# Kernel tuning notes

Hardware: AMD Instinct MI355X
Metric: run time of the kernel (lower is better)

Reference implementation:

```python
import jax, jax.numpy as jnp
import numpy as np

B, SY, SX, CIN = 16, 180, 360, 16
WIDTH, MODES = 32, 32


def _vandermonde(pos, modes):
    # Nonuniform DFT matrix V[k, n] = exp(-2*pi*i * k * p_n) / sqrt(L),
    # positions normalized to [0, 1). Inverse uses conj(V) (near-unitary).
    p = (pos - pos.min()) / (pos.max() - pos.min())
    k = jnp.arange(modes, dtype=jnp.float32)
    V = jnp.exp(-2j * jnp.pi * k[:, None] * p[None, :]) / jnp.sqrt(jnp.float32(pos.shape[0]))
    return V.astype(jnp.complex64)


def _spectral(h, fw1, fw2, Vy, Vx):
    # h: [B, C, M, N]; Vy: [modes, M]; Vx: [modes, N]
    hc = h.astype(jnp.complex64)
    w1 = fw1[..., 0] + 1j * fw1[..., 1]  # [I, O, modes] complex
    w2 = fw2[..., 0] + 1j * fw2[..., 1]
    # y-direction: forward transform over M, mix channels per mode, inverse
    fty = jnp.einsum('bimn,km->bink', hc, Vy)          # [B, I, N, modes]
    oy = jnp.einsum('bink,iok->bonk', fty, w1)          # [B, O, N, modes]
    xy = jnp.einsum('bonk,km->bomn', oy, jnp.conj(Vy)).real
    # x-direction: forward transform over N
    ftx = jnp.einsum('bimn,kn->bimk', hc, Vx)           # [B, I, M, modes]
    ox = jnp.einsum('bimk,iok->bomk', ftx, w2)          # [B, O, M, modes]
    xx = jnp.einsum('bomk,kn->bomn', ox, jnp.conj(Vx)).real
    return xx + xy


def gelu(v):
    return jax.nn.gelu(v, approximate=False)  # torch F.gelu default (erf)


def setup_inputs() -> dict:
    key = jax.random.key(0)
    ks = jax.random.split(key, 16)
    s = 1.0 / (WIDTH * WIDTH)
    return {
        'x': jax.random.normal(ks[0], (B, SY, SX, CIN), jnp.float32),
        'sparse_x': jnp.sort(jax.random.uniform(ks[1], (SX,), jnp.float32)),
        'sparse_y': jnp.sort(jax.random.uniform(ks[2], (SY,), jnp.float32)),
        'fc0_w': jax.random.normal(ks[3], (CIN + 2, WIDTH), jnp.float32) * 0.1,
        'fc0_b': jnp.zeros((WIDTH,), jnp.float32),
        'fw1': jax.random.uniform(ks[4], (4, WIDTH, WIDTH, MODES, 2), jnp.float32) * s,
        'fw2': jax.random.uniform(ks[5], (4, WIDTH, WIDTH, MODES, 2), jnp.float32) * s,
        'w1': jax.random.normal(ks[6], (4, WIDTH, WIDTH), jnp.float32) * 0.1,
        'b1': jnp.zeros((4, WIDTH), jnp.float32),
        'w2': jax.random.normal(ks[7], (4, WIDTH, WIDTH), jnp.float32) * 0.1,
        'b2': jnp.zeros((4, WIDTH), jnp.float32),
        'fc1_w': jax.random.normal(ks[8], (WIDTH, 128), jnp.float32) * 0.1,
        'fc1_b': jnp.zeros((128,), jnp.float32),
        'fc2_w': jax.random.normal(ks[9], (128, 1), jnp.float32) * 0.1,
        'fc2_b': jnp.zeros((1,), jnp.float32),
    }


def reference(x, sparse_x, sparse_y, fc0_w, fc0_b, fw1, fw2, w1, b1, w2, b2,
              fc1_w, fc1_b, fc2_w, fc2_b):
    b, sy, sx, _ = x.shape
    # get_grid (faithful to source: (p - min)/max)
    gx = (sparse_x - sparse_x.min()) / sparse_x.max()          # [SX]
    gy = (sparse_y - sparse_y.min()) / sparse_y.max()          # [SY]
    grid = jnp.stack([jnp.broadcast_to(gx[None, :], (sy, sx)),
                      jnp.broadcast_to(gy[:, None], (sy, sx))], axis=-1)
    grid = jnp.broadcast_to(grid[None], (b, sy, sx, 2))
    h = jnp.concatenate([x, grid], axis=-1) @ fc0_w + fc0_b    # [B, SY, SX, W]
    h = jnp.transpose(h, (0, 3, 1, 2))                         # [B, W, SY, SX]

    Vy = _vandermonde(sparse_y, MODES)
    Vx = _vandermonde(sparse_x, MODES)

    for i in range(4):
        x1 = _spectral(h, fw1[i], fw2[i], Vy, Vx)
        x2 = jnp.einsum('bcmn,oc->bomn', x1, w1[i]) + b1[i][None, :, None, None]
        x4 = jnp.einsum('bcmn,oc->bomn', gelu(x2), w2[i]) + b2[i][None, :, None, None]
        h = (gelu(x4) if i < 3 else x4) + h  # last block: no gelu on x4 (per source)

    h = jnp.transpose(h, (0, 2, 3, 1))                         # [B, SY, SX, W]
    h = gelu(h @ fc1_w + fc1_b)
    return h @ fc2_w + fc2_b                                   # [B, SY, SX, 1]
```

## Files before the change

### kernel.cpp

```cpp
#include <hip/hip_runtime.h>
#include <math.h>

#define NB 16
#define NSY 180
#define NSX 360
#define NCIN 16
#define NW 32
#define NMODES 32
#define NPIX (NSY*NSX)
#define NPTS (NB*NPIX)

typedef unsigned int uint;
typedef unsigned short ushort;
typedef __attribute__((ext_vector_type(8))) short bf16x8;
typedef __attribute__((ext_vector_type(4))) float f32x4;

union U4 { uint u[4]; bf16x8 v; };

__device__ __forceinline__ float gelu_f(float v){
  float u = v*(-2.3021681f - 0.10295335f*v*v);
  return v * __builtin_amdgcn_rcpf(1.f + exp2f(u));
}
__device__ __forceinline__ ushort f2bf(float x){
  uint u = __float_as_uint(x);
  return (ushort)((u + 0x7FFFu + ((u>>16)&1u)) >> 16);
}
__device__ __forceinline__ uint packbf2(float a, float b){
  return (uint)f2bf(a) | ((uint)f2bf(b) << 16);
}
__device__ __forceinline__ float bf2f(ushort u){
  return __uint_as_float(((uint)u) << 16);
}
__device__ __forceinline__ uint addbf2(uint h, uint a){
  return packbf2(bf2f((ushort)(h & 0xffffu)) + bf2f((ushort)(a & 0xffffu)),
                 bf2f((ushort)(h >> 16))     + bf2f((ushort)(a >> 16)));
}

__global__ __launch_bounds__(256) void k_prep(const float* __restrict__ sx,
    const float* __restrict__ sy, const float* __restrict__ fc1_w,
    const float* __restrict__ w2m,
    ushort* __restrict__ Abfy, ushort* __restrict__ Abfx,
    ushort* __restrict__ VyCT, ushort* __restrict__ VxCT,
    ushort* __restrict__ f1Tbf, ushort* __restrict__ w2bf,
    float* __restrict__ gx, float* __restrict__ gy){
  int idx = blockIdx.x*256 + threadIdx.x;
  float sx0 = sx[0], sxL = sx[NSX-1];
  float sy0 = sy[0], syL = sy[NSY-1];
  const float scy = 0.07453559924999298980f;
  const float scx = 0.05270462766947298886f;
  if (idx < NSX) gx[idx] = (sx[idx]-sx0)/sxL;
  if (idx < NSY) gy[idx] = (sy[idx]-sy0)/syL;
  if (idx < 64*192){
    int kri = idx/192, m = idx%192;
    float val = 0.f;
    if (m < NSY){
      int k = kri>>1;
      float p = (sy[m]-sy0)/(syL-sy0);
      float ang = -6.2831853071795864769f*(float)k*p;
      val = ((kri&1)? sinf(ang) : cosf(ang))*scy;
    }
    Abfy[idx] = f2bf(val);
  }
  if (idx < 192*64){
    int m = idx/64, kri = idx%64;
    float val = 0.f;
    if (m < NSY){
      int k = kri>>1;
      float p = (sy[m]-sy0)/(syL-sy0);
      float ang = -6.2831853071795864769f*(float)k*p;
      val = ((kri&1)? sinf(ang) : cosf(ang))*scy;
    }
    VyCT[idx] = f2bf(val);
  }
  if (idx < 64*384){
    int kri = idx/384, n = idx%384;
    float val = 0.f;
    if (n < NSX){
      int k = kri>>1;
      float p = (sx[n]-sx0)/(sxL-sx0);
      float ang = -6.2831853071795864769f*(float)k*p;
      val = ((kri&1)? sinf(ang) : cosf(ang))*scx;
    }
    Abfx[idx] = f2bf(val);
  }
  if (idx < 384*64){
    int n = idx/64, kri = idx%64;
    float val = 0.f;
    if (n < NSX){
      int k = kri>>1;
      float p = (sx[n]-sx0)/(sxL-sx0);
      float ang = -6.2831853071795864769f*(float)k*p;
      val = ((kri&1)? sinf(ang) : cosf(ang))*scx;
    }
    VxCT[idx] = f2bf(val);
  }
  if (idx < 128*32){
    int j = idx >> 5, c = idx & 31;
    f1Tbf[idx] = f2bf(fc1_w[c*128 + j]);
  }
  if (idx < 4096){
    w2bf[idx] = f2bf(w2m[idx]);
  }
}

__global__ __launch_bounds__(256) void k_fold(const float* __restrict__ fw1,
    const float* __restrict__ fw2, const float* __restrict__ w1m,
    float* __restrict__ w1f, float* __restrict__ w2f){
  int id = blockIdx.x*256 + threadIdx.x;
  int half = id >> 17;
  int r = id & 131071;
  int i  = r >> 15;
  int in = (r >> 10) & 31;
  int k  = (r >> 5) & 31;
  int o  = r & 31;
  const float* src = half ? fw2 : fw1;
  const float* wm  = w1m + i*1024 + o*32;
  const float* sp  = src + ((size_t)((i*32+in)*1024 + k))*2;
  float sR = 0.f, sI = 0.f;
  #pragma unroll
  for (int c=0;c<32;c++){
    float w = wm[c];
    sR += w * sp[c*64];
    sI += w * sp[c*64+1];
  }
  float* dst = half ? w2f : w1f;
  size_t oi = ((size_t)((i*32+in)*32 + k)*32 + o)*2;
  dst[oi] = sR; dst[oi+1] = sI;
}

__global__ __launch_bounds__(256) void k_fc0(const float* __restrict__ x,
    const float* __restrict__ gx, const float* __restrict__ gy,
    const float* __restrict__ fw, const float* __restrict__ fb,
    ushort* __restrict__ hbf){
  int p = blockIdx.x*256 + threadIdx.x;
  if (p >= NPTS) return;
  int b = p/NPIX, r = p%NPIX, m = r/NSX, n = r%NSX;
  const float* xp = x + (size_t)p*NCIN;
  float xv[NCIN+2];
  #pragma unroll
  for (int j=0;j<NCIN;j++) xv[j] = xp[j];
  xv[16] = gx[n]; xv[17] = gy[m];
  float acc[NW];
  #pragma unroll
  for (int o=0;o<NW;o++) acc[o] = fb[o];
  #pragma unroll
  for (int j=0;j<NCIN+2;j++){
    float v = xv[j];
    #pragma unroll
    for (int o=0;o<NW;o++) acc[o] += v*fw[j*32+o];
  }
  ushort* hq = hbf + (size_t)b*NW*NPIX + r;
  #pragma unroll
  for (int o=0;o<NW;o++) hq[(size_t)o*NPIX] = f2bf(acc[o]);
}

__global__ __launch_bounds__(256) void k_fwd(const ushort* __restrict__ hbf,
    const ushort* __restrict__ Abfy, const ushort* __restrict__ Abfx,
    uint* __restrict__ fty, uint* __restrict__ ftx, int b0, int ylim){
  __shared__ ushort rawS[2][32*64];
  __shared__ uint   BtS[2][64*18];
  int bx = blockIdx.x;
  int tid = threadIdx.x;
  int l = tid & 63, g = tid >> 6;
  int c15 = l & 15, q = l >> 4;
  if (bx < ylim){
    int nt6 = bx % 6; int c = (bx/6) & 31; int bb = bx/192;
    int n0 = nt6*64;
    const ushort* hb = hbf + (size_t)((b0+bb)*NW + c)*NPIX;
    int yr = tid >> 3, yc = (tid & 7) << 3;
    auto ldY = [&](int ks)->uint4{
      int m = ks*32 + yr;
      int gc = n0 + yc;
      uint4 p = {0u,0u,0u,0u};
      if (m < NSY && gc < NSX) p = *(const uint4*)(hb + (size_t)m*NSX + gc);
      return p;
    };
    bf16x8 afr[6];
    #pragma unroll
    for (int ks=0; ks<6; ks++)
      afr[ks] = *(const bf16x8*)(Abfy + (size_t)(16*g + c15)*192 + ks*32 + q*8);
    f32x4 acc[4];
    #pragma unroll
    for (int t=0;t<4;t++) acc[t] = (f32x4){0.f,0.f,0.f,0.f};
    uint4 pre0 = ldY(0);
    uint4 pre1 = ldY(1);
    #pragma unroll
    for (int ks=0; ks<6; ks++){
      uint4 cur = (ks&1) ? pre1 : pre0;
      *(uint4*)(&rawS[ks&1][(size_t)tid*8]) = cur;
      __syncthreads();
      if (ks < 4){
        if (ks&1) pre1 = ldY(ks+2); else pre0 = ldY(ks+2);
      }
      const ushort* rp = rawS[ks&1];
      ushort v[8];
      #pragma unroll
      for (int j=0;j<8;j++) v[j] = rp[(8*g + j)*64 + l];
      #pragma unroll
      for (int i=0;i<4;i++)
        BtS[ks&1][l*18 + 4*g + i] = (uint)v[2*i] | ((uint)v[2*i+1] << 16);
      __syncthreads();
      #pragma unroll
      for (int nt=0; nt<4; nt++){
        const uint* bp = &BtS[ks&1][(nt*16 + c15)*18 + q*4];
        U4 bu;
        uint2 lo = *(const uint2*)(bp);
        uint2 hi = *(const uint2*)(bp+2);
        bu.u[0]=lo.x; bu.u[1]=lo.y; bu.u[2]=hi.x; bu.u[3]=hi.y;
        acc[nt] = __builtin_amdgcn_mfma_f32_16x16x32_bf16(afr[ks], bu.v, acc[nt], 0,0,0);
      }
    }
    uint* fb = fty + (size_t)(bb*NW + c)*32*NSX;
    int k0 = 8*g + 2*q;
    #pragma unroll
    for (int nt=0; nt<4; nt++){
      int nn = n0 + nt*16 + c15;
      if (nn < NSX){
        fb[(size_t)k0*NSX + nn]     = packbf2(acc[nt][0], acc[nt][1]);
        fb[(size_t)(k0+1)*NSX + nn] = packbf2(acc[nt][2], acc[nt][3]);
      }
    }
  } else {
    int t = bx - ylim;
    int mt = t % 3; int c = (t/3) & 31; int bb = t/96;
    int m0 = mt*64;
    const ushort* hb = hbf + (size_t)((b0+bb)*NW + c)*NPIX;
    int xr = tid >> 2, xc = (tid & 3) << 3;
    auto ldX = [&](int ks)->uint4{
      int m = m0 + xr;
      int n = ks*32 + xc;
      uint4 p = {0u,0u,0u,0u};
      if (m < NSY && n < NSX) p = *(const uint4*)(hb + (size_t)m*NSX + n);
      return p;
    };
    auto ldA = [&](int ks)->bf16x8{
      return *(const bf16x8*)(Abfx + (size_t)(16*g + c15)*384 + ks*32 + q*8);
    };
    f32x4 acc[4];
    #pragma unroll
    for (int tt=0;tt<4;tt++) acc[tt] = (f32x4){0.f,0.f,0.f,0.f};
    uint4 pre0 = ldX(0), pre1 = ldX(1);
    bf16x8 a0 = ldA(0), a1 = ldA(1);
    int s4 = (tid & 3) * 4;
    #pragma unroll
    for (int ks=0; ks<12; ks++){
      uint4 cur = (ks&1) ? pre1 : pre0;
      bf16x8 af = (ks&1) ? a1 : a0;
      uint* btp = &BtS[ks&1][xr*18 + s4];
      btp[0] = cur.x; btp[1] = cur.y; btp[2] = cur.z; btp[3] = cur.w;
      if (ks < 10){
        if (ks&1){ pre1 = ldX(ks+2); a1 = ldA(ks+2); }
        else     { pre0 = ldX(ks+2); a0 = ldA(ks+2); }
      }
      __syncthreads();
      #pragma unroll
      for (int nt=0; nt<4; nt++){
        const uint* bp = &BtS[ks&1][(nt*16 + c15)*18 + q*4];
        U4 bu;
        uint2 lo = *(const uint2*)(bp);
        uint2 hi = *(const uint2*)(bp+2);
        bu.u[0]=lo.x; bu.u[1]=lo.y; bu.u[2]=hi.x; bu.u[3]=hi.y;
        acc[nt] = __builtin_amdgcn_mfma_f32_16x16x32_bf16(af, bu.v, acc[nt], 0,0,0);
      }
    }
    uint* fb = ftx + (size_t)(bb*NW + c)*32*NSY;
    int k0 = 8*g + 2*q;
    #pragma unroll
    for (int nt=0; nt<4; nt++){
      int mm = m0 + nt*16 + c15;
      if (mm < NSY){
        fb[(size_t)k0*NSY + mm]     = packbf2(acc[nt][0], acc[nt][1]);
        fb[(size_t)(k0+1)*NSY + mm] = packbf2(acc[nt][2], acc[nt][3]);
      }
    }
  }
}

__global__ __launch_bounds__(192) void k_mix(const uint* __restrict__ fty,
    const uint* __restrict__ ftx, const float* __restrict__ w1f,
    const float* __restrict__ w2f, uint* __restrict__ oy, uint* __restrict__ ox,
    int ylim){
  int bx = blockIdx.x;
  const uint* ft; const float* wf; uint* oo; int Nlen, k, bb, n;
  if (bx < ylim){
    int t = bx; int nt = t & 1; k = (t>>1) & 31; bb = t >> 6;
    n = nt*192 + threadIdx.x; ft = fty; wf = w1f; oo = oy; Nlen = NSX;
  } else {
    int t = bx - ylim; k = t & 31; bb = t >> 5;
    n = threadIdx.x; ft = ftx; wf = w2f; oo = ox; Nlen = NSY;
  }
  bool valid = n < Nlen;
  int nn = valid ? n : (Nlen-1);
  const uint* fb = ft + ((size_t)(bb*NW)*32 + k)*Nlen + nn;
  const float* wb = wf + (size_t)k*64;
  float aR[32], aI[32];
  #pragma unroll
  for (int o=0;o<32;o++){ aR[o]=0.f; aI[o]=0.f; }
  for (int in=0; in<32; in++){
    uint f = fb[(size_t)in*32*Nlen];
    float fR = bf2f((ushort)(f & 0xffffu));
    float fI = bf2f((ushort)(f >> 16));
    const float* wrow = wb + in*2048;
    #pragma unroll
    for (int o=0;o<32;o++){
      float wR = wrow[o*2], wI = wrow[o*2+1];
      aR[o] += fR*wR - fI*wI;
      aI[o] += fR*wI + fI*wR;
    }
  }
  if (valid){
    uint* ob = oo + ((size_t)(bb*NW)*32 + k)*Nlen + n;
    #pragma unroll
    for (int o=0;o<32;o++){
      ob[(size_t)o*32*Nlen] = packbf2(aR[o], aI[o]);
    }
  }
}

__global__ __launch_bounds__(256) void k_inv(const uint* __restrict__ oyb,
    const uint* __restrict__ oxb, const ushort* __restrict__ VyCT,
    const ushort* __restrict__ VxCT, const float* __restrict__ b1,
    ushort* __restrict__ x2bf){
  __shared__ uint Bt[64*34];
  int bx = blockIdx.x;
  int c8 = bx & 7; int rr = bx >> 3; int slot = rr/6; int nt6 = rr - slot*6;
  int gid = slot*8 + c8;
  int bb = gid >> 5; int o = gid & 31;
  int n0 = nt6*64;
  int tid = threadIdx.x;
  int l = tid & 63, g = tid >> 6;
  int c15 = l & 15, q = l >> 4;
  const uint* oxp = oxb + (size_t)(bb*NW + o)*32*NSY;
  const uint* oyp = oyb + (size_t)(bb*NW + o)*32*NSX;
  #pragma unroll
  for (int i=0;i<8;i++){
    int idx = tid + i*256;
    int k = idx >> 6, n = idx & 63;
    int ng = n0 + n;
    Bt[n*34 + k] = (ng < NSX) ? oyp[(size_t)k*NSX + ng] : 0u;
  }
  __syncthreads();
  f32x4 acc[3][4];
  #pragma unroll
  for (int mt=0;mt<3;mt++)
    #pragma unroll
    for (int nt=0;nt<4;nt++) acc[mt][nt] = (f32x4){0.f,0.f,0.f,0.f};
  #pragma unroll
  for (int s=0;s<4;s++){
    bf16x8 bfr[4];
    #pragma unroll
    for (int nt=0;nt<4;nt++){
      if (s < 2){
        const uint* bp = &Bt[(nt*16 + c15)*34 + s*16 + q*4];
        U4 bu; uint2 lo = *(const uint2*)bp; uint2 hi = *(const uint2*)(bp+2);
        bu.u[0]=lo.x; bu.u[1]=lo.y; bu.u[2]=hi.x; bu.u[3]=hi.y;
        bfr[nt] = bu.v;
      } else {
        bfr[nt] = *(const bf16x8*)(VxCT + (size_t)(n0 + nt*16 + c15)*64 + (s-2)*32 + q*8);
      }
    }
    #pragma unroll
    for (int mt=0;mt<3;mt++){
      int mrow = g*48 + mt*16 + c15;
      bf16x8 afr;
      if (s < 2){
        afr = *(const bf16x8*)(VyCT + (size_t)mrow*64 + s*32 + q*8);
      } else {
        int mc = mrow < NSY ? mrow : (NSY-1);
        int k0 = (s-2)*16 + q*4;
        U4 au;
        #pragma unroll
        for (int j=0;j<4;j++)
          au.u[j] = oxp[(size_t)(k0+j)*NSY + mc];
        afr = au.v;
      }
      #pragma unroll
      for (int nt=0;nt<4;nt++)
        acc[mt][nt] = __builtin_amdgcn_mfma_f32_16x16x32_bf16(afr, bfr[nt], acc[mt][nt], 0,0,0);
    }
  }
  float bias = b1[o];
  ushort* xp = x2bf + (size_t)(bb*NW + o)*NPIX;
  #pragma unroll
  for (int mt=0;mt<3;mt++){
    #pragma unroll
    for (int nt=0;nt<4;nt++){
      int n = n0 + nt*16 + c15;
      if (n < NSX){
        #pragma unroll
        for (int r2=0;r2<4;r2++){
          int m = g*48 + mt*16 + q*4 + r2;
          if (m < NSY) xp[(size_t)m*NSX + n] = f2bf(gelu_f(acc[mt][nt][r2] + bias));
        }
      }
    }
  }
}

__global__ __launch_bounds__(256) void k_pw2(const ushort* __restrict__ x2bf,
    const ushort* __restrict__ w2b, const float* __restrict__ b2,
    uint* __restrict__ hbfu, int b0, int nloc){
  const int HP = NPIX/2;
  __shared__ uint Ot[32*132];
  int blk = blockIdx.x;
  int bb = blk/254, bt = blk - bb*254;
  int pxb = bt*256;
  int tid = threadIdx.x;
  int g = tid >> 6, l = tid & 63;
  int c15 = l & 15, q = l >> 4;
  bf16x8 bfr[2];
  #pragma unroll
  for (int nt=0; nt<2; nt++)
    bfr[nt] = *(const bf16x8*)(w2b + (size_t)(nt*16 + c15)*32 + q*8);
  const ushort* xb = x2bf + ((size_t)bb*NW + q*8)*NPIX;
  f32x4 acc[4][2];
  #pragma unroll
  for (int mt=0;mt<4;mt++){
    U4 au; au.u[0]=0u; au.u[1]=0u; au.u[2]=0u; au.u[3]=0u;
    int pr = pxb + g*64 + mt*16 + c15;
    if (pr < NPIX){
      ushort v[8];
      #pragma unroll
      for (int j=0;j<8;j++) v[j] = xb[(size_t)j*NPIX + pr];
      #pragma unroll
      for (int i2=0;i2<4;i2++) au.u[i2] = (uint)v[2*i2] | ((uint)v[2*i2+1] << 16);
    }
    #pragma unroll
    for (int nt=0;nt<2;nt++){
      acc[mt][nt] = (f32x4){0.f,0.f,0.f,0.f};
      acc[mt][nt] = __builtin_amdgcn_mfma_f32_16x16x32_bf16(au.v, bfr[nt], acc[mt][nt], 0,0,0);
    }
  }
  #pragma unroll
  for (int nt=0;nt<2;nt++){
    int o = nt*16 + c15;
    float bias = b2[o];
    #pragma unroll
    for (int mt=0;mt<4;mt++){
      float v0 = gelu_f(acc[mt][nt][0] + bias);
      float v1 = gelu_f(acc[mt][nt][1] + bias);
      float v2 = gelu_f(acc[mt][nt][2] + bias);
      float v3 = gelu_f(acc[mt][nt][3] + bias);
      int px2 = g*32 + mt*8 + q*2;
      uint2 w2v; w2v.x = packbf2(v0,v1); w2v.y = packbf2(v2,v3);
      *(uint2*)(&Ot[o*132 + px2]) = w2v;
    }
  }
  __syncthreads();
  int o = tid >> 3, t8 = tid & 7;
  uint* hb = hbfu + ((size_t)((b0+bb)*NW + o))*HP + (pxb>>1) + t8*16;
  const uint* lrow = &Ot[o*132 + t8*16];
  int p2g0 = (pxb>>1) + t8*16;
  #pragma unroll
  for (int jj=0; jj<16; jj+=4){
    if (p2g0 + jj + 4 <= HP){
      uint4 hv = *(const uint4*)(hb + jj);
      uint4 av = *(const uint4*)(lrow + jj);
      uint4 r;
      r.x = addbf2(hv.x, av.x); r.y = addbf2(hv.y, av.y);
      r.z = addbf2(hv.z, av.z); r.w = addbf2(hv.w, av.w);
      *(uint4*)(hb + jj) = r;
    } else {
      #pragma unroll
      for (int t=0;t<4;t++){
        if (p2g0 + jj + t < HP){
          uint hv = hb[jj+t];
          hb[jj+t] = addbf2(hv, lrow[jj+t]);
        }
      }
    }
  }
}

__global__ __launch_bounds__(256) void k_pw2f(const ushort* __restrict__ x2bf,
    const ushort* __restrict__ w2b, const float* __restrict__ b2,
    const uint* __restrict__ hbfu,
    const ushort* __restrict__ f1Tbf, const float* __restrict__ f1b,
    const float* __restrict__ f2w, const float* __restrict__ f2b,
    float* __restrict__ out, int b0){
  const int HP = NPIX/2;
  __shared__ uint Ot[32*132];
  int blk = blockIdx.x;
  int bb = blk/254, bt = blk - bb*254;
  int pxb = bt*256;
  int tid = threadIdx.x;
  int g = tid >> 6, l = tid & 63;
  int c15 = l & 15, q = l >> 4;
  bf16x8 bfr[2];
  #pragma unroll
  for (int nt=0; nt<2; nt++)
    bfr[nt] = *(const bf16x8*)(w2b + (size_t)(nt*16 + c15)*32 + q*8);
  const ushort* xb = x2bf + ((size_t)bb*NW + q*8)*NPIX;
  f32x4 acc[4][2];
  #pragma unroll
  for (int mt=0;mt<4;mt++){
    U4 au; au.u[0]=0u; au.u[1]=0u; au.u[2]=0u; au.u[3]=0u;
    int pr = pxb + g*64 + mt*16 + c15;
    if (pr < NPIX){
      ushort v[8];
      #pragma unroll
      for (int j=0;j<8;j++) v[j] = xb[(size_t)j*NPIX + pr];
      #pragma unroll
      for (int i2=0;i2<4;i2++) au.u[i2] = (uint)v[2*i2] | ((uint)v[2*i2+1] << 16);
    }
    #pragma unroll
    for (int nt=0;nt<2;nt++){
      acc[mt][nt] = (f32x4){0.f,0.f,0.f,0.f};
      acc[mt][nt] = __builtin_amdgcn_mfma_f32_16x16x32_bf16(au.v, bfr[nt], acc[mt][nt], 0,0,0);
    }
  }
  #pragma unroll
  for (int nt=0;nt<2;nt++){
    int o = nt*16 + c15;
    float bias = b2[o];
    #pragma unroll
    for (int mt=0;mt<4;mt++){
      float v0 = acc[mt][nt][0] + bias;
      float v1 = acc[mt][nt][1] + bias;
      float v2 = acc[mt][nt][2] + bias;
      float v3 = acc[mt][nt][3] + bias;
      int px2 = g*32 + mt*8 + q*2;
      uint2 w2v; w2v.x = packbf2(v0,v1); w2v.y = packbf2(v2,v3);
      *(uint2*)(&Ot[o*132 + px2]) = w2v;
    }
  }
  __syncthreads();
  {
    int o = tid >> 3, t8 = tid & 7;
    const uint* hb = hbfu + ((size_t)((b0+bb)*NW + o))*HP + (pxb>>1) + t8*16;
    uint* lrow = &Ot[o*132 + t8*16];
    int p2g0 = (pxb>>1) + t8*16;
    #pragma unroll
    for (int jj=0; jj<16; jj+=4){
      if (p2g0 + jj + 4 <= HP){
        uint4 hv = *(const uint4*)(hb + jj);
        lrow[jj+0] = addbf2(hv.x, lrow[jj+0]);
        lrow[jj+1] = addbf2(hv.y, lrow[jj+1]);
        lrow[jj+2] = addbf2(hv.z, lrow[jj+2]);
        lrow[jj+3] = addbf2(hv.w, lrow[jj+3]);
      } else {
        #pragma unroll
        for (int t=0;t<4;t++){
          if (p2g0 + jj + t < HP)
            lrow[jj+t] = addbf2(hb[jj+t], lrow[jj+t]);
        }
      }
    }
  }
  bf16x8 b1fr[8];
  #pragma unroll
  for (int nt=0; nt<8; nt++)
    b1fr[nt] = *(const bf16x8*)(f1Tbf + (size_t)(nt*16 + c15)*32 + q*8);
  __syncthreads();
  const ushort* Ts = (const ushort*)Ot;
  float fb2 = f2b[0];
  float* ob = out + (size_t)(b0+bb)*NPIX + pxb;
  #pragma unroll
  for (int mt=0;mt<4;mt++){
    int px_in = g*64 + mt*16 + c15;
    const ushort* tp = Ts + (size_t)(q*8)*264 + px_in;
    ushort v[8];
    #pragma unroll
    for (int j2=0;j2<8;j2++) v[j2] = tp[j2*264];
    U4 au;
    #pragma unroll
    for (int i2=0;i2<4;i2++) au.u[i2] = (uint)v[2*i2] | ((uint)v[2*i2+1] << 16);
    f32x4 a8[8];
    #pragma unroll
    for (int nt=0; nt<8; nt++){
      a8[nt] = (f32x4){0.f,0.f,0.f,0.f};
      a8[nt] = __builtin_amdgcn_mfma_f32_16x16x32_bf16(au.v, b1fr[nt], a8[nt], 0,0,0);
    }
    float s[4] = {0.f,0.f,0.f,0.f};
    #pragma unroll
    for (int nt=0; nt<8; nt++){
      int jj = nt*16 + c15;
      float bj = f1b[jj], wj = f2w[jj];
      #pragma unroll
      for (int r2=0;r2<4;r2++) s[r2] += gelu_f(a8[nt][r2] + bj) * wj;
    }
    #pragma unroll
    for (int msk=1; msk<16; msk<<=1){
      #pragma unroll
      for (int r2=0;r2<4;r2++) s[r2] += __shfl_xor(s[r2], msk, 64);
    }
    if (c15 == 0){
      int pl = g*64 + mt*16 + q*4;
      if (pxb + pl + 4 <= NPIX){
        float4 o4 = {s[0]+fb2, s[1]+fb2, s[2]+fb2, s[3]+fb2};
        *(float4*)(ob + pl) = o4;
      }
    }
  }
}

extern "C" void kernel_launch(void* const* d_in, const int* in_sizes, int n_in,
                              void* d_out, int out_size, void* d_ws, size_t ws_size,
                              hipStream_t stream) {
  const float* x     = (const float*)d_in[0];
  const float* sx    = (const float*)d_in[1];
  const float* sy    = (const float*)d_in[2];
  const float* fc0_w = (const float*)d_in[3];
  const float* fc0_b = (const float*)d_in[4];
  const float* fw1   = (const float*)d_in[5];
  const float* fw2   = (const float*)d_in[6];
  const float* w1m   = (const float*)d_in[7];
  const float* b1    = (const float*)d_in[8];
  const float* w2m   = (const float*)d_in[9];
  const float* b2    = (const float*)d_in[10];
  const float* fc1_w = (const float*)d_in[11];
  const float* fc1_b = (const float*)d_in[12];
  const float* fc2_w = (const float*)d_in[13];
  const float* fc2_b = (const float*)d_in[14];
  float* out = (float*)d_out;

  char* wsb = (char*)d_ws;
  size_t off = 0;
  auto alloc = [&](size_t bytes)->char*{
    char* p = wsb + off;
    off = (off + bytes + 255) & ~(size_t)255;
    return p;
  };
  ushort* hbf   = (ushort*)alloc((size_t)NB*NW*NPIX*2);
  ushort* Abfy  = (ushort*)alloc(64*192*2);
  ushort* Abfx  = (ushort*)alloc(64*384*2);
  ushort* VyCT  = (ushort*)alloc(192*64*2);
  ushort* VxCT  = (ushort*)alloc(384*64*2);
  ushort* f1Tbf = (ushort*)alloc(128*32*2);
  ushort* w2bf  = (ushort*)alloc(4096*2);
  float*  gx    = (float*)alloc(NSX*4);
  float*  gy    = (float*)alloc(NSY*4);
  float*  w1f   = (float*)alloc(262144*4);
  float*  w2f   = (float*)alloc(262144*4);
  const size_t fixedB = off;

  const size_t szX2  = (size_t)NW*NPIX*2;
  const size_t szFty = (size_t)NW*32*NSX*4;
  const size_t szFtx = (size_t)NW*32*NSY*4;
  const size_t szOy  = szFty, szOx = szFtx;
  const size_t perB  = szX2 + szOy + szOx;

  int NC = 16;
  while (NC > 1 && fixedB + (size_t)NC*perB + 4096 > ws_size) NC >>= 1;
  char* pb = wsb + fixedB;
  ushort* x2bf = (ushort*)pb;
  uint*   fty  = (uint*)pb;
  uint*   ftx  = (uint*)(pb + (size_t)NC*szFty);
  uint*   oy   = (uint*)(pb + (size_t)NC*szX2);
  uint*   ox   = (uint*)((char*)oy + (size_t)NC*szOy);

  k_prep<<<96, 256, 0, stream>>>(sx, sy, fc1_w, w2m, Abfy, Abfx, VyCT, VxCT,
                                 f1Tbf, w2bf, gx, gy);
  k_fold<<<1024, 256, 0, stream>>>(fw1, fw2, w1m, w1f, w2f);
  k_fc0<<<4050, 256, 0, stream>>>(x, gx, gy, fc0_w, fc0_b, hbf);

  for (int i=0;i<4;i++){
    for (int b0=0; b0<NB; b0+=NC){
      k_fwd<<<NC*288, 256, 0, stream>>>(hbf, Abfy, Abfx, fty, ftx, b0, NC*192);
      k_mix<<<NC*96, 192, 0, stream>>>(fty, ftx, w1f + (size_t)i*65536,
                                       w2f + (size_t)i*65536, oy, ox, NC*64);
      k_inv<<<NC*192, 256, 0, stream>>>(oy, ox, VyCT, VxCT, b1 + i*32, x2bf);
      if (i < 3){
        k_pw2<<<NC*254, 256, 0, stream>>>((const ushort*)x2bf,
                                          w2bf + (size_t)i*1024,
                                          b2 + i*32, (uint*)hbf, b0, NC);
      } else {
        k_pw2f<<<NC*254, 256, 0, stream>>>((const ushort*)x2bf,
                                           w2bf + (size_t)i*1024,
                                           b2 + i*32, (const uint*)hbf,
                                           f1Tbf, fc1_b, fc2_w, fc2_b,
                                           out, b0);
      }
    }
  }
}
```

Before: 921.3 us.

## Run spectral channel mixing on bf16 MFMA with split hi/lo weights

Replaces the scalar FP32 complex channel-mix kernel with an MFMA version. The folded weights are pre-packed into bf16 hi/lo pairs arranged as real-valued 2x2 complex blocks, so the mix becomes bf16 matrix multiplies with error-compensated weights. Each block handles all N positions for one (batch, mode) and prefetches the next tile. This is meant to remove the heavy FP32 FMA cost of the per-pixel loops. In exchange it doubles the MFMA count to recover weight precision and changes the weight layout and the launch geometry.

```diff
diff --git a/kernel.cpp b/kernel.cpp
--- a/kernel.cpp
+++ b/kernel.cpp
@@ -105,7 +105,7 @@
 
 __global__ __launch_bounds__(256) void k_fold(const float* __restrict__ fw1,
     const float* __restrict__ fw2, const float* __restrict__ w1m,
-    float* __restrict__ w1f, float* __restrict__ w2f){
+    ushort* __restrict__ wAbf){
   int id = blockIdx.x*256 + threadIdx.x;
   int half = id >> 17;
   int r = id & 131071;
@@ -123,9 +123,15 @@
     sR += w * sp[c*64];
     sI += w * sp[c*64+1];
   }
-  float* dst = half ? w2f : w1f;
-  size_t oi = ((size_t)((i*32+in)*32 + k)*32 + o)*2;
-  dst[oi] = sR; dst[oi+1] = sI;
+  ushort rH = f2bf(sR);  ushort rL = f2bf(sR - bf2f(rH));
+  ushort iH = f2bf(sI);  ushort iL = f2bf(sI - bf2f(iH));
+  ushort nH = f2bf(-sI); ushort nL = f2bf(-sI - bf2f(nH));
+  ushort* base = wAbf + (((size_t)((i*2 + half)*32 + k)) << 13);
+  int oi = o*64 + 2*in;
+  base[oi]          = rH;  base[oi+1]        = nH;
+  base[2048 + oi]   = rL;  base[2048 + oi+1] = nL;
+  base[4096 + oi]   = iH;  base[4096 + oi+1] = rH;
+  base[6144 + oi]   = iL;  base[6144 + oi+1] = rL;
 }
 
 __global__ __launch_bounds__(256) void k_fc0(const float* __restrict__ x,
@@ -276,43 +282,73 @@
   }
 }
 
-__global__ __launch_bounds__(192) void k_mix(const uint* __restrict__ fty,
-    const uint* __restrict__ ftx, const float* __restrict__ w1f,
-    const float* __restrict__ w2f, uint* __restrict__ oy, uint* __restrict__ ox,
-    int ylim){
+__global__ __launch_bounds__(256) void k_mix2(const uint* __restrict__ fty,
+    const uint* __restrict__ ftx, const ushort* __restrict__ wA,
+    uint* __restrict__ oy, uint* __restrict__ ox, int ylim){
   int bx = blockIdx.x;
-  const uint* ft; const float* wf; uint* oo; int Nlen, k, bb, n;
+  const uint* ft; uint* oo; int Nlen, NT, k, bb, halfoff;
   if (bx < ylim){
-    int t = bx; int nt = t & 1; k = (t>>1) & 31; bb = t >> 6;
-    n = nt*192 + threadIdx.x; ft = fty; wf = w1f; oo = oy; Nlen = NSX;
+    bb = bx >> 5; k = bx & 31; ft = fty; oo = oy; Nlen = NSX; NT = 23; halfoff = 0;
   } else {
-    int t = bx - ylim; k = t & 31; bb = t >> 5;
-    n = threadIdx.x; ft = ftx; wf = w2f; oo = ox; Nlen = NSY;
-  }
-  bool valid = n < Nlen;
-  int nn = valid ? n : (Nlen-1);
-  const uint* fb = ft + ((size_t)(bb*NW)*32 + k)*Nlen + nn;
-  const float* wb = wf + (size_t)k*64;
-  float aR[32], aI[32];
-  #pragma unroll
-  for (int o=0;o<32;o++){ aR[o]=0.f; aI[o]=0.f; }
-  for (int in=0; in<32; in++){
-    uint f = fb[(size_t)in*32*Nlen];
-    float fR = bf2f((ushort)(f & 0xffffu));
-    float fI = bf2f((ushort)(f >> 16));
-    const float* wrow = wb + in*2048;
-    #pragma unroll
-    for (int o=0;o<32;o++){
-      float wR = wrow[o*2], wI = wrow[o*2+1];
-      aR[o] += fR*wR - fI*wI;
-      aI[o] += fR*wI + fI*wR;
-    }
-  }
-  if (valid){
-    uint* ob = oo + ((size_t)(bb*NW)*32 + k)*Nlen + n;
-    #pragma unroll
-    for (int o=0;o<32;o++){
-      ob[(size_t)o*32*Nlen] = packbf2(aR[o], aI[o]);
+    int t = bx - ylim;
+    bb = t >> 5; k = t & 31; ft = ftx; oo = ox; Nlen = NSY; NT = 12; halfoff = 262144;
+  }
+  int tid = threadIdx.x;
+  int g = tid >> 6, l = tid & 63;
+  int c15 = l & 15, q = l >> 4;
+  const ushort* wk = wA + halfoff + k*8192;
+  bf16x8 af[2][2][2][2];
+  #pragma unroll
+  for (int mt=0;mt<2;mt++)
+    #pragma unroll
+    for (int s=0;s<2;s++)
+      #pragma unroll
+      for (int ps=0;ps<2;ps++)
+        #pragma unroll
+        for (int pr=0;pr<2;pr++)
+          af[mt][s][ps][pr] = *(const bf16x8*)(wk + ps*4096 + pr*2048
+                                               + (mt*16+c15)*64 + s*32 + q*8);
+  const uint* fb = ft + ((size_t)bb*1024 + (size_t)k)*Nlen;
+  uint* ob = oo + ((size_t)bb*1024 + (size_t)k)*Nlen;
+  auto ldB = [&](int nt, U4* bu){
+    int n = nt*16 + c15; if (n >= Nlen) n = Nlen-1;
+    #pragma unroll
+    for (int s=0;s<2;s++)
+      #pragma unroll
+      for (int t=0;t<4;t++){
+        int in = s*16 + q*4 + t;
+        bu[s].u[t] = fb[(size_t)in*32*Nlen + n];
+      }
+  };
+  U4 pre[2], cur[2];
+  ldB(g, pre);
+  for (int nt = g; nt < NT; nt += 4){
+    cur[0] = pre[0]; cur[1] = pre[1];
+    if (nt + 4 < NT) ldB(nt+4, pre);
+    f32x4 acc[2][2];
+    #pragma unroll
+    for (int mt=0;mt<2;mt++)
+      #pragma unroll
+      for (int ps=0;ps<2;ps++)
+        acc[mt][ps] = (f32x4){0.f,0.f,0.f,0.f};
+    #pragma unroll
+    for (int s=0;s<2;s++)
+      #pragma unroll
+      for (int mt=0;mt<2;mt++)
+        #pragma unroll
+        for (int ps=0;ps<2;ps++){
+          acc[mt][ps] = __builtin_amdgcn_mfma_f32_16x16x32_bf16(af[mt][s][ps][0], cur[s].v, acc[mt][ps], 0,0,0);
+          acc[mt][ps] = __builtin_amdgcn_mfma_f32_16x16x32_bf16(af[mt][s][ps][1], cur[s].v, acc[mt][ps], 0,0,0);
+        }
+    int n = nt*16 + c15;
+    if (n < Nlen){
+      #pragma unroll
+      for (int mt=0;mt<2;mt++)
+        #pragma unroll
+        for (int r2=0;r2<4;r2++){
+          int o = mt*16 + q*4 + r2;
+          ob[(size_t)o*32*Nlen + n] = packbf2(acc[mt][0][r2], acc[mt][1][r2]);
+        }
     }
   }
 }
@@ -630,8 +666,7 @@
   ushort* w2bf  = (ushort*)alloc(4096*2);
   float*  gx    = (float*)alloc(NSX*4);
   float*  gy    = (float*)alloc(NSY*4);
-  float*  w1f   = (float*)alloc(262144*4);
-  float*  w2f   = (float*)alloc(262144*4);
+  ushort* wAbf  = (ushort*)alloc((size_t)4*2*32*4*2048*2);
   const size_t fixedB = off;
 
   const size_t szX2  = (size_t)NW*NPIX*2;
@@ -651,14 +686,14 @@
 
   k_prep<<<96, 256, 0, stream>>>(sx, sy, fc1_w, w2m, Abfy, Abfx, VyCT, VxCT,
                                  f1Tbf, w2bf, gx, gy);
-  k_fold<<<1024, 256, 0, stream>>>(fw1, fw2, w1m, w1f, w2f);
+  k_fold<<<1024, 256, 0, stream>>>(fw1, fw2, w1m, wAbf);
   k_fc0<<<4050, 256, 0, stream>>>(x, gx, gy, fc0_w, fc0_b, hbf);
 
   for (int i=0;i<4;i++){
     for (int b0=0; b0<NB; b0+=NC){
       k_fwd<<<NC*288, 256, 0, stream>>>(hbf, Abfy, Abfx, fty, ftx, b0, NC*192);
-      k_mix<<<NC*96, 192, 0, stream>>>(fty, ftx, w1f + (size_t)i*65536,
-                                       w2f + (size_t)i*65536, oy, ox, NC*64);
+      k_mix2<<<NC*64, 256, 0, stream>>>(fty, ftx, wAbf + (size_t)i*524288,
+                                        oy, ox, NC*32);
       k_inv<<<NC*192, 256, 0, stream>>>(oy, ox, VyCT, VxCT, b1 + i*32, x2bf);
       if (i < 3){
         k_pw2<<<NC*254, 256, 0, stream>>>((const ushort*)x2bf,
```

New measurement: 806.3 us. -12.5%, faster.
